# Kernel tuning notes

Hardware: AMD Instinct MI355X
Metric: run time of the kernel (lower is better)

Reference implementation:

```python
import jax, jax.numpy as jnp
import numpy as np

D = 256          # d_model
NH = 8           # n_heads
HD = D // NH
LEV = 3          # n_levels
NP = 4           # n_points
DFF = 1024       # d_ffn
B = 8            # batch
LQ = 3600        # 60*60 queries (hardcoded in get_reference_points)
SHAPES = np.array([[60, 60], [30, 30], [15, 15]], dtype=np.int64)
LIN = int((SHAPES[:, 0] * SHAPES[:, 1]).sum())  # 4725
START = np.concatenate([[0], np.cumsum(SHAPES[:, 0] * SHAPES[:, 1])[:-1]]).astype(np.int64)


def setup_inputs() -> dict:
    key = jax.random.key(0)
    ks = iter(jax.random.split(key, 32))
    def lin(k, o, i):
        return jax.random.normal(k, (o, i), jnp.float32) * 0.02
    return {
        "tgt": jax.random.normal(next(ks), (LQ, B, D), jnp.float32),
        "query_pos": jax.random.normal(next(ks), (1, 1, D), jnp.float32),
        "src": jax.random.normal(next(ks), (B, LIN, D), jnp.float32),
        "src_spatial_shapes": jnp.asarray(SHAPES),
        "level_start_index": jnp.asarray(START),
        "in_proj_w": lin(next(ks), 3 * D, D),
        "in_proj_b": jnp.zeros((3 * D,), jnp.float32),
        "out_proj_w": lin(next(ks), D, D),
        "out_proj_b": jnp.zeros((D,), jnp.float32),
        "samp_off_w": lin(next(ks), NH * LEV * NP * 2, D),
        "samp_off_b": jax.random.normal(next(ks), (NH * LEV * NP * 2,), jnp.float32) * 0.5,
        "attn_w_w": lin(next(ks), NH * LEV * NP, D),
        "attn_w_b": jnp.zeros((NH * LEV * NP,), jnp.float32),
        "value_proj_w": lin(next(ks), D, D),
        "value_proj_b": jnp.zeros((D,), jnp.float32),
        "cross_out_w": lin(next(ks), D, D),
        "cross_out_b": jnp.zeros((D,), jnp.float32),
        "ln1_g": jnp.ones((D,), jnp.float32), "ln1_b": jnp.zeros((D,), jnp.float32),
        "ln2_g": jnp.ones((D,), jnp.float32), "ln2_b": jnp.zeros((D,), jnp.float32),
        "ln3_g": jnp.ones((D,), jnp.float32), "ln3_b": jnp.zeros((D,), jnp.float32),
        "ffn_w1": lin(next(ks), DFF, D), "ffn_b1": jnp.zeros((DFF,), jnp.float32),
        "ffn_w2": lin(next(ks), D, DFF), "ffn_b2": jnp.zeros((D,), jnp.float32),
    }


def _ln(x, g, b, eps=1e-5):
    m = x.mean(-1, keepdims=True)
    v = ((x - m) ** 2).mean(-1, keepdims=True)
    return (x - m) * jax.lax.rsqrt(v + eps) * g + b


def _self_attn(q_in, k_in, v_in, wqkv, bqkv, wo, bo):
    # torch nn.MultiheadAttention semantics, inputs laid out (seq, batch, embed)
    S, N, _ = q_in.shape
    q = (q_in @ wqkv[:D].T + bqkv[:D]).reshape(S, N, NH, HD)
    k = (k_in @ wqkv[D:2 * D].T + bqkv[D:2 * D]).reshape(S, N, NH, HD)
    v = (v_in @ wqkv[2 * D:].T + bqkv[2 * D:]).reshape(S, N, NH, HD)
    logits = jnp.einsum('snhd,tnhd->nhst', q, k) / np.sqrt(HD).astype(np.float32)
    a = jax.nn.softmax(logits, -1)
    ctx = jnp.einsum('nhst,tnhd->snhd', a, v).reshape(S, N, D)
    return ctx @ wo.T + bo


def _bilinear(v_l, loc, Hl, Wl):
    # v_l: [B, NH, Hl*Wl, HD]; loc: [B, NH, LQ, NP, 2] normalized in [0,1]
    # grid_sample(align_corners=False, padding=zeros): pixel = loc*size - 0.5
    x = loc[..., 0] * Wl - 0.5
    y = loc[..., 1] * Hl - 0.5
    x0 = jnp.floor(x); y0 = jnp.floor(y)
    fx = x - x0; fy = y - y0
    x0 = x0.astype(jnp.int32); y0 = y0.astype(jnp.int32)
    def corner(yi, xi, w):
        valid = ((xi >= 0) & (xi < Wl) & (yi >= 0) & (yi < Hl)).astype(v_l.dtype)
        idx = jnp.clip(yi, 0, Hl - 1) * Wl + jnp.clip(xi, 0, Wl - 1)
        b, h, lq, p = idx.shape
        g = jnp.take_along_axis(v_l, idx.reshape(b, h, lq * p)[..., None], axis=2)
        return g.reshape(b, h, lq, p, HD) * (w * valid)[..., None]
    return (corner(y0, x0, (1 - fx) * (1 - fy))
            + corner(y0, x0 + 1, fx * (1 - fy))
            + corner(y0 + 1, x0, (1 - fx) * fy)
            + corner(y0 + 1, x0 + 1, fx * fy))


def _msdeform(query, ref, src, wso, bso, waw, baw, wv, bv, wo, bo):
    Bq, Lq, _ = query.shape
    value = (src @ wv.T + bv).reshape(Bq, LIN, NH, HD).transpose(0, 2, 1, 3)  # [B,NH,LIN,HD]
    off = (query @ wso.T + bso).reshape(Bq, Lq, NH, LEV, NP, 2)
    aw = (query @ waw.T + baw).reshape(Bq, Lq, NH, LEV * NP)
    aw = jax.nn.softmax(aw, -1).reshape(Bq, Lq, NH, LEV, NP)
    normalizer = jnp.asarray(SHAPES[:, ::-1].copy(), jnp.float32)  # (W, H) per level
    loc = ref[:, :, None, :, None, :] + off / normalizer[None, None, None, :, None, :]
    out = jnp.zeros((Bq, NH, Lq, HD), query.dtype)
    for l in range(LEV):
        Hl, Wl = int(SHAPES[l, 0]), int(SHAPES[l, 1])
        s = int(START[l])
        v_l = value[:, :, s:s + Hl * Wl]
        loc_l = loc[:, :, :, l].transpose(0, 2, 1, 3, 4)      # [B,NH,LQ,NP,2]
        sampled = _bilinear(v_l, loc_l, Hl, Wl)               # [B,NH,LQ,NP,HD]
        out = out + (sampled * aw[:, :, :, l].transpose(0, 2, 1, 3)[..., None]).sum(3)
    out = out.transpose(0, 2, 1, 3).reshape(Bq, Lq, D)
    return out @ wo.T + bo


def _reference_points():
    Hh = Ww = 60
    ys = (jnp.arange(Hh, dtype=jnp.float32) + 0.5) / Hh
    xs = (jnp.arange(Ww, dtype=jnp.float32) + 0.5) / Ww
    yy, xx = jnp.meshgrid(ys, xs, indexing='ij')
    ref = jnp.stack([xx.reshape(-1), yy.reshape(-1)], -1)[None]  # [1, 3600, 2]
    return jnp.broadcast_to(ref[:, :, None, :], (1, Hh * Ww, LEV, 2))


def reference(tgt, query_pos, src, src_spatial_shapes, level_start_index,
              in_proj_w, in_proj_b, out_proj_w, out_proj_b,
              samp_off_w, samp_off_b, attn_w_w, attn_w_b,
              value_proj_w, value_proj_b, cross_out_w, cross_out_b,
              ln1_g, ln1_b, ln2_g, ln2_b, ln3_g, ln3_b,
              ffn_w1, ffn_b1, ffn_w2, ffn_b2):
    # dropout layers are identity (eval mode). spatial shapes are static metadata
    # (SHAPES/START) since slicing sizes must be static under jit.
    q = (tgt + query_pos).transpose(1, 0, 2)
    tgt2 = _self_attn(q, q, tgt.transpose(1, 0, 2), in_proj_w, in_proj_b, out_proj_w, out_proj_b)
    t = _ln(tgt + tgt2.transpose(1, 0, 2), ln2_g, ln2_b)
    ref = _reference_points()
    tq = t.transpose(1, 0, 2)  # permute(1,0,2) -> [B, LQ, D]
    tgt2 = _msdeform(tq + query_pos, ref, src, samp_off_w, samp_off_b,
                     attn_w_w, attn_w_b, value_proj_w, value_proj_b,
                     cross_out_w, cross_out_b)
    tq = _ln(tq + tgt2, ln1_g, ln1_b)
    ff = jax.nn.relu(tq @ ffn_w1.T + ffn_b1) @ ffn_w2.T + ffn_b2
    tq = _ln(tq + ff, ln3_g, ln3_b)
    return tq.transpose(1, 0, 2)  # [LQ, B, D]
```

## Files before the change

kernel.cpp:

```cpp
#include <hip/hip_runtime.h>
#include <hip/hip_bf16.h>
#include <cstddef>
#include <cstdint>

#define D_MODEL 256
#define NHEAD   8
#define HDIM    32
#define NLEV    3
#define NPNT    4
#define DFF     1024
#define BATCH   8
#define LQ      3600
#define LIN     4725
#define MROWS   (BATCH*LQ)

typedef short bf16x8 __attribute__((ext_vector_type(8)));
typedef float f32x4  __attribute__((ext_vector_type(4)));

__device__ __forceinline__ unsigned short f2b(float x) {
    unsigned int u = __float_as_uint(x);
    unsigned int r = (u + 0x7fffu + ((u >> 16) & 1u)) >> 16;
    return (unsigned short)r;
}
__device__ __forceinline__ float b2f(unsigned short s) {
    return __uint_as_float(((unsigned int)s) << 16);
}

#define GLDS16(g, l) __builtin_amdgcn_global_load_lds( \
    (const __attribute__((address_space(1))) void*)(g), \
    (__attribute__((address_space(3))) void*)(l), 16, 0, 0)

#define WTOT 991232
__global__ __launch_bounds__(256) void prep_kernel(
    const float* __restrict__ tgt, unsigned short* __restrict__ tgtb,
    const float* __restrict__ srcf, unsigned short* __restrict__ srcb,
    const float* __restrict__ w_in, const float* __restrict__ w_out,
    const float* __restrict__ w_val, const float* __restrict__ w_cross,
    const float* __restrict__ w_so, const float* __restrict__ w_aw,
    const float* __restrict__ w_f1, const float* __restrict__ w_f2,
    unsigned short* __restrict__ wdst,
    const float* __restrict__ qp, const float* __restrict__ so_b,
    const float* __restrict__ aw_b, float* __restrict__ qpv)
{
    const int bid = blockIdx.x;
    const int tid = threadIdx.x;
    if (bid < 7200) {
        int i = bid * 256 + tid;
        float4 v = ((const float4*)tgt)[i];
        ushort4 o; o.x = f2b(v.x); o.y = f2b(v.y); o.z = f2b(v.z); o.w = f2b(v.w);
        ((ushort4*)tgtb)[i] = o;
    } else if (bid < 16650) {
        int i = (bid - 7200) * 256 + tid;
        float4 v = ((const float4*)srcf)[i];
        ushort4 o; o.x = f2b(v.x); o.y = f2b(v.y); o.z = f2b(v.z); o.w = f2b(v.w);
        ((ushort4*)srcb)[i] = o;
    } else if (bid < 17618) {
        int idx = ((bid - 16650) * 256 + tid) * 4;
        if (idx >= WTOT) return;
        const float* src; int off;
        if      (idx < 196608) { src = w_in;    off = idx; }
        else if (idx < 262144) { src = w_out;   off = idx - 196608; }
        else if (idx < 327680) { src = w_val;   off = idx - 262144; }
        else if (idx < 393216) { src = w_cross; off = idx - 327680; }
        else if (idx < 442368) { src = w_so;    off = idx - 393216; }
        else if (idx < 466944) { src = w_aw;    off = idx - 442368; }
        else if (idx < 729088) { src = w_f1;    off = idx - 466944; }
        else                   { src = w_f2;    off = idx - 729088; }
        float4 v = *(const float4*)(src + off);
        ushort4 o; o.x = f2b(v.x); o.y = f2b(v.y); o.z = f2b(v.z); o.w = f2b(v.w);
        *(ushort4*)(wdst + idx) = o;
    } else {
        int o = (bid - 17618) * 256 + tid;
        if (o >= 768 + 192 + 96) return;
        const float* wrow;
        if (o < 768)       wrow = w_in + (size_t)o * D_MODEL;
        else if (o < 960)  wrow = w_so + (size_t)(o - 768) * D_MODEL;
        else               wrow = w_aw + (size_t)(o - 960) * D_MODEL;
        float acc = 0.f;
        for (int d = 0; d < D_MODEL; ++d) acc += qp[d] * wrow[d];
        qpv[o] = acc;
        if (o >= 768) {
            float bias = (o < 960) ? so_b[o - 768] : aw_b[o - 960];
            qpv[1056 + (o - 768)] = acc + bias;
        }
    }
}

__global__ __launch_bounds__(256) void gemm_bf16(
    const unsigned short* __restrict__ A,
    const unsigned short* __restrict__ W,
    const float* __restrict__ bias,
    const float* __restrict__ bias2, int b2lim,
    float* __restrict__ Cf, unsigned short* __restrict__ Cb,
    int M, int N, int K, int relu)
{
    __shared__ __align__(16) unsigned short As[2 * 128 * 32];
    __shared__ __align__(16) unsigned short Bs[2 * 128 * 32];
    const int tid  = threadIdx.x;
    const int wave = tid >> 6;
    const int lane = tid & 63;
    const int m0 = blockIdx.x * 128;
    const int n0 = blockIdx.y * 128;

    const int lr  = lane >> 2;
    const int lc8 = (lane & 3) * 8;
    int ar0 = m0 + wave * 32 + lr;      if (ar0 > M - 1) ar0 = M - 1;
    int ar1 = m0 + wave * 32 + 16 + lr; if (ar1 > M - 1) ar1 = M - 1;
    int br0 = n0 + wave * 32 + lr;      if (br0 > N - 1) br0 = N - 1;
    int br1 = n0 + wave * 32 + 16 + lr; if (br1 > N - 1) br1 = N - 1;
    const unsigned short* pa0 = A + (size_t)ar0 * K + lc8;
    const unsigned short* pa1 = A + (size_t)ar1 * K + lc8;
    const unsigned short* pb0 = W + (size_t)br0 * K + lc8;
    const unsigned short* pb1 = W + (size_t)br1 * K + lc8;
    unsigned short* la0 = As + wave * 1024;
    unsigned short* la1 = As + wave * 1024 + 512;
    unsigned short* lb0 = Bs + wave * 1024;
    unsigned short* lb1 = Bs + wave * 1024 + 512;

    const int wm = (wave >> 1) * 64;
    const int wn = (wave & 1) * 64;
    const int fr = lane & 15;
    const int fk = (lane >> 4) * 8;

    f32x4 acc[4][4] = {};

    for (int k0 = 0; k0 < K; k0 += 64) {
        GLDS16(pa0, la0); GLDS16(pa0 + 32, la0 + 4096);
        GLDS16(pa1, la1); GLDS16(pa1 + 32, la1 + 4096);
        GLDS16(pb0, lb0); GLDS16(pb0 + 32, lb0 + 4096);
        GLDS16(pb1, lb1); GLDS16(pb1 + 32, lb1 + 4096);
        pa0 += 64; pa1 += 64; pb0 += 64; pb1 += 64;
        __syncthreads();
#pragma unroll
        for (int p = 0; p < 2; ++p) {
            bf16x8 af[4], bfv[4];
#pragma unroll
            for (int i = 0; i < 4; ++i)
                af[i] = *(const bf16x8*)&As[p * 4096 + (wm + i * 16 + fr) * 32 + fk];
#pragma unroll
            for (int j = 0; j < 4; ++j)
                bfv[j] = *(const bf16x8*)&Bs[p * 4096 + (wn + j * 16 + fr) * 32 + fk];
#pragma unroll
            for (int i = 0; i < 4; ++i)
#pragma unroll
                for (int j = 0; j < 4; ++j)
                    acc[i][j] = __builtin_amdgcn_mfma_f32_16x16x32_bf16(
                        af[i], bfv[j], acc[i][j], 0, 0, 0);
        }
        __syncthreads();
    }

    const int quad = lane >> 4;
#pragma unroll
    for (int j = 0; j < 4; ++j) {
        const int col = n0 + wn + j * 16 + fr;
        if (col >= N) continue;
        float bv = 0.f;
        if (bias) bv += bias[col];
        if (bias2 && col < b2lim) bv += bias2[col];
#pragma unroll
        for (int i = 0; i < 4; ++i) {
#pragma unroll
            for (int r = 0; r < 4; ++r) {
                const int row = m0 + wm + i * 16 + quad * 4 + r;
                if (row >= M) continue;
                float v = acc[i][j][r] + bv;
                if (relu) v = fmaxf(v, 0.f);
                if (Cf) Cf[(size_t)row * N + col] = v;
                if (Cb) Cb[(size_t)row * N + col] = f2b(v);
            }
        }
    }
}

__global__ __launch_bounds__(256) void gemm_ln(
    const unsigned short* __restrict__ A,
    const unsigned short* __restrict__ W,
    const float* __restrict__ bias,
    const float* __restrict__ resid,
    const float* __restrict__ g, const float* __restrict__ bb,
    float* __restrict__ outf, unsigned short* __restrict__ outb, int K)
{
    __shared__ __align__(16) unsigned short As[2 * 64 * 32];
    __shared__ __align__(16) unsigned short Bs[2 * 256 * 32];
    const int tid  = threadIdx.x;
    const int wave = tid >> 6;
    const int lane = tid & 63;
    const int m0 = blockIdx.x * 64;

    const int arow = tid >> 2;
    const int akc  = (tid & 3) * 8;
    const unsigned short* pa = A + (size_t)(m0 + arow) * K + akc;
    unsigned short* la = As + tid * 8;
    const unsigned short* pb0 = W + (size_t)(arow)       * K + akc;
    const unsigned short* pb1 = W + (size_t)(64  + arow) * K + akc;
    const unsigned short* pb2 = W + (size_t)(128 + arow) * K + akc;
    const unsigned short* pb3 = W + (size_t)(192 + arow) * K + akc;
    unsigned short* lb0 = Bs + tid * 8;
    unsigned short* lb1 = Bs + 2048 + tid * 8;
    unsigned short* lb2 = Bs + 4096 + tid * 8;
    unsigned short* lb3 = Bs + 6144 + tid * 8;

    const int fr = lane & 15;
    const int fk = (lane >> 4) * 8;
    const int quad = lane >> 4;
    const int colbase = wave * 64;

    f32x4 acc[4][4] = {};

    for (int k0 = 0; k0 < K; k0 += 64) {
        GLDS16(pa, la);        GLDS16(pa + 32, la + 2048);
        GLDS16(pb0, lb0);      GLDS16(pb0 + 32, lb0 + 8192);
        GLDS16(pb1, lb1);      GLDS16(pb1 + 32, lb1 + 8192);
        GLDS16(pb2, lb2);      GLDS16(pb2 + 32, lb2 + 8192);
        GLDS16(pb3, lb3);      GLDS16(pb3 + 32, lb3 + 8192);
        pa += 64; pb0 += 64; pb1 += 64; pb2 += 64; pb3 += 64;
        __syncthreads();
#pragma unroll
        for (int p = 0; p < 2; ++p) {
            bf16x8 af[4], bfv[4];
#pragma unroll
            for (int i = 0; i < 4; ++i)
                af[i] = *(const bf16x8*)&As[p * 2048 + (i * 16 + fr) * 32 + fk];
#pragma unroll
            for (int j = 0; j < 4; ++j)
                bfv[j] = *(const bf16x8*)&Bs[p * 8192 + (colbase + j * 16 + fr) * 32 + fk];
#pragma unroll
            for (int i = 0; i < 4; ++i)
#pragma unroll
                for (int j = 0; j < 4; ++j)
                    acc[i][j] = __builtin_amdgcn_mfma_f32_16x16x32_bf16(
                        af[i], bfv[j], acc[i][j], 0, 0, 0);
        }
        __syncthreads();
    }

    float2* red = (float2*)As;
    float rs[4][4], rq[4][4];
#pragma unroll
    for (int i = 0; i < 4; ++i) {
#pragma unroll
        for (int r = 0; r < 4; ++r) {
            const int row = m0 + i * 16 + quad * 4 + r;
            float s = 0.f, q = 0.f;
#pragma unroll
            for (int j = 0; j < 4; ++j) {
                const int col = colbase + j * 16 + fr;
                float v = acc[i][j][r] + bias[col] + resid[(size_t)row * 256 + col];
                acc[i][j][r] = v;
                s += v; q += v * v;
            }
            rs[i][r] = s; rq[i][r] = q;
        }
    }
#pragma unroll
    for (int off = 1; off < 16; off <<= 1) {
#pragma unroll
        for (int i = 0; i < 4; ++i)
#pragma unroll
            for (int r = 0; r < 4; ++r) {
                rs[i][r] += __shfl_xor(rs[i][r], off);
                rq[i][r] += __shfl_xor(rq[i][r], off);
            }
    }
    if ((lane & 15) == 0) {
#pragma unroll
        for (int i = 0; i < 4; ++i)
#pragma unroll
            for (int r = 0; r < 4; ++r)
                red[wave * 64 + i * 16 + quad * 4 + r] = make_float2(rs[i][r], rq[i][r]);
    }
    __syncthreads();
#pragma unroll
    for (int i = 0; i < 4; ++i) {
#pragma unroll
        for (int r = 0; r < 4; ++r) {
            const int rl = i * 16 + quad * 4 + r;
            const float2 t0 = red[rl], t1 = red[64 + rl], t2 = red[128 + rl], t3 = red[192 + rl];
            const float sum = t0.x + t1.x + t2.x + t3.x;
            const float sq  = t0.y + t1.y + t2.y + t3.y;
            const float mean = sum * (1.f / 256.f);
            const float var  = sq * (1.f / 256.f) - mean * mean;
            const float inv  = rsqrtf(var + 1e-5f);
            const int row = m0 + rl;
#pragma unroll
            for (int j = 0; j < 4; ++j) {
                const int col = colbase + j * 16 + fr;
                const float val = (acc[i][j][r] - mean) * inv * g[col] + bb[col];
                outf[(size_t)row * 256 + col] = val;
                if (outb) outb[(size_t)row * 256 + col] = f2b(val);
            }
        }
    }
}

__global__ __launch_bounds__(256) void self_attn_kernel(
    const unsigned short* __restrict__ qkv, unsigned short* __restrict__ ctx)
{
    __shared__ float sh[8][768];
    __shared__ float ls[8][8][8];
    const int n = blockIdx.x;
    const int t = threadIdx.x;
#pragma unroll
    for (int s = 0; s < 8; ++s) {
        const unsigned short* row = qkv + (size_t)(n * 8 + s) * 768;
        sh[s][t]       = b2f(row[t]);
        sh[s][t + 256] = b2f(row[t + 256]);
        sh[s][t + 512] = b2f(row[t + 512]);
    }
    __syncthreads();
    const int h = t >> 5, j = t & 31;
#pragma unroll
    for (int pair = j; pair < 64; pair += 32) {
        const int s = pair >> 3, tt = pair & 7;
        float acc = 0.f;
#pragma unroll
        for (int d = 0; d < 32; ++d)
            acc += sh[s][h * 32 + d] * sh[tt][256 + h * 32 + d];
        ls[h][s][tt] = acc * 0.17677669529663687f;
    }
    __syncthreads();
    if (t < 64) {
        const int hh = t >> 3, s = t & 7;
        float mx = -1e30f;
        for (int tt = 0; tt < 8; ++tt) mx = fmaxf(mx, ls[hh][s][tt]);
        float sum = 0.f;
        for (int tt = 0; tt < 8; ++tt) { float e = expf(ls[hh][s][tt] - mx); ls[hh][s][tt] = e; sum += e; }
        const float inv = 1.f / sum;
        for (int tt = 0; tt < 8; ++tt) ls[hh][s][tt] *= inv;
    }
    __syncthreads();
#pragma unroll
    for (int s = 0; s < 8; ++s) {
        float acc = 0.f;
#pragma unroll
        for (int tt = 0; tt < 8; ++tt)
            acc += ls[h][s][tt] * sh[tt][512 + h * 32 + j];
        ctx[(size_t)(n * 8 + s) * D_MODEL + h * 32 + j] = f2b(acc);
    }
}

__global__ __launch_bounds__(256) void msprep_kernel(float* __restrict__ comb)
{
    const int tid = threadIdx.x;
    const int m = blockIdx.x * 32 + (tid >> 3);
    const int h = tid & 7;
    const int lq = m >> 3;
    const float* offp = comb + (size_t)m * 288 + h * 24;
    const float* awp  = comb + (size_t)m * 288 + 192 + h * 12;
    float off[24], aw[12];
#pragma unroll
    for (int i = 0; i < 6; ++i) *(float4*)&off[i * 4] = ((const float4*)offp)[i];
#pragma unroll
    for (int i = 0; i < 3; ++i) *(float4*)&aw[i * 4] = ((const float4*)awp)[i];

    float mx = aw[0];
#pragma unroll
    for (int i = 1; i < 12; ++i) mx = fmaxf(mx, aw[i]);
    float se = 0.f;
#pragma unroll
    for (int i = 0; i < 12; ++i) { aw[i] = __expf(aw[i] - mx); se += aw[i]; }
    const float inv = 1.f / se;

    const float refx = ((lq % 60) + 0.5f) * (1.f / 60.f);
    const float refy = ((lq / 60) + 0.5f) * (1.f / 60.f);
    const int HW[3] = {60, 30, 15};
    const int ST[3] = {0, 3600, 4500};

    unsigned int outv[36];
#pragma unroll
    for (int lev = 0; lev < NLEV; ++lev) {
        const int Wl = HW[lev], Hl = HW[lev], s0 = ST[lev];
        const float fWl = (float)Wl, fHl = (float)Hl;
#pragma unroll
        for (int p = 0; p < NPNT; ++p) {
            const int pt = lev * 4 + p;
            const float ox = off[lev * 8 + p * 2];
            const float oy = off[lev * 8 + p * 2 + 1];
            const float px = refx * fWl + ox - 0.5f;
            const float py = refy * fHl + oy - 0.5f;
            const float x0f = floorf(px), y0f = floorf(py);
            const float fx = px - x0f, fy = py - y0f;
            const int x0 = (int)x0f, y0 = (int)y0f;
            const float aww = aw[pt] * inv;
            const float vx0 = (x0 >= 0 && x0 < Wl) ? 1.f : 0.f;
            const float vx1 = (x0 >= -1 && x0 < Wl - 1) ? 1.f : 0.f;
            const float vy0 = (y0 >= 0 && y0 < Hl) ? 1.f : 0.f;
            const float vy1 = (y0 >= -1 && y0 < Hl - 1) ? 1.f : 0.f;
            const int xc0 = min(max(x0, 0), Wl - 1);
            const int xc1 = min(max(x0 + 1, 0), Wl - 1);
            const int yc0 = min(max(y0, 0), Hl - 1);
            const int yc1 = min(max(y0 + 1, 0), Hl - 1);
            const unsigned int sx  = (unsigned int)(xc1 - xc0);
            const unsigned int syW = (unsigned int)((yc1 - yc0) * Wl);
            const unsigned int idx = (unsigned int)(s0 + yc0 * Wl + xc0);
            const float w00 = (1.f - fx) * (1.f - fy) * aww * vx0 * vy0;
            const float w01 = fx * (1.f - fy) * aww * vx1 * vy0;
            const float w10 = (1.f - fx) * fy * aww * vx0 * vy1;
            const float w11 = fx * fy * aww * vx1 * vy1;
            outv[pt * 3]     = idx | (sx << 16) | (syW << 17);
            outv[pt * 3 + 1] = (unsigned int)f2b(w00) | ((unsigned int)f2b(w01) << 16);
            outv[pt * 3 + 2] = (unsigned int)f2b(w10) | ((unsigned int)f2b(w11) << 16);
        }
    }
    __syncthreads();
    uint4* dst = (uint4*)((char*)comb + (size_t)m * 1152 + h * 144);
#pragma unroll
    for (int i = 0; i < 9; ++i) dst[i] = *(uint4*)&outv[i * 4];
}

__global__ __launch_bounds__(256) void msdeform_kernel(
    const unsigned short* __restrict__ value,
    const unsigned int* __restrict__ meta,
    unsigned short* __restrict__ out)
{
    const int bid = blockIdx.x;
    const int b   = bid & 7;
    const int lq0 = (bid >> 3) * 4;
    const int r    = threadIdx.x >> 6;
    const int lane = threadIdx.x & 63;
    const int h = lane >> 3;
    const int l = lane & 7;
    const int m = (lq0 + r) * 8 + b;

    const unsigned int* mp = meta + (size_t)m * 288 + h * 36;
    uint4 md[9];
#pragma unroll
    for (int i = 0; i < 9; ++i) md[i] = ((const uint4*)mp)[i];
    const unsigned int* mw = (const unsigned int*)md;

    const unsigned short* vbase = value + (size_t)b * LIN * 256 + h * 32 + l * 4;

    float a0 = 0.f, a1 = 0.f, a2 = 0.f, a3 = 0.f;
#pragma unroll
    for (int p = 0; p < 12; ++p) {
        const unsigned int pack = mw[p * 3];
        const unsigned int wlo  = mw[p * 3 + 1];
        const unsigned int whi  = mw[p * 3 + 2];
        const unsigned int i00 = pack & 0xFFFFu;
        const unsigned int sx  = (pack >> 16) & 1u;
        const unsigned int syW = pack >> 17;
        const unsigned int i01 = i00 + sx;
        const unsigned int i10 = i00 + syW;
        const unsigned int i11 = i10 + sx;
        const float w00 = __uint_as_float(wlo << 16);
        const float w01 = __uint_as_float(wlo & 0xFFFF0000u);
        const float w10 = __uint_as_float(whi << 16);
        const float w11 = __uint_as_float(whi & 0xFFFF0000u);
        const ushort4 g00 = *(const ushort4*)(vbase + (size_t)i00 * 256);
        const ushort4 g01 = *(const ushort4*)(vbase + (size_t)i01 * 256);
        const ushort4 g10 = *(const ushort4*)(vbase + (size_t)i10 * 256);
        const ushort4 g11 = *(const ushort4*)(vbase + (size_t)i11 * 256);
        a0 += b2f(g00.x) * w00 + b2f(g01.x) * w01 + b2f(g10.x) * w10 + b2f(g11.x) * w11;
        a1 += b2f(g00.y) * w00 + b2f(g01.y) * w01 + b2f(g10.y) * w10 + b2f(g11.y) * w11;
        a2 += b2f(g00.z) * w00 + b2f(g01.z) * w01 + b2f(g10.z) * w10 + b2f(g11.z) * w11;
        a3 += b2f(g00.w) * w00 + b2f(g01.w) * w01 + b2f(g10.w) * w10 + b2f(g11.w) * w11;
    }
    ushort4 o;
    o.x = f2b(a0); o.y = f2b(a1); o.z = f2b(a2); o.w = f2b(a3);
    *(ushort4*)(out + (size_t)m * 256 + h * 32 + l * 4) = o;
}

extern "C" void kernel_launch(void* const* d_in, const int* in_sizes, int n_in,
                              void* d_out, int out_size, void* d_ws, size_t ws_size,
                              hipStream_t stream)
{
    (void)in_sizes; (void)n_in; (void)out_size; (void)ws_size;
    const float* tgt          = (const float*)d_in[0];
    const float* qp           = (const float*)d_in[1];
    const float* src          = (const float*)d_in[2];
    const float* in_proj_w    = (const float*)d_in[5];
    const float* in_proj_b    = (const float*)d_in[6];
    const float* out_proj_w   = (const float*)d_in[7];
    const float* out_proj_b   = (const float*)d_in[8];
    const float* samp_off_w   = (const float*)d_in[9];
    const float* samp_off_b   = (const float*)d_in[10];
    const float* attn_w_w     = (const float*)d_in[11];
    const float* attn_w_b     = (const float*)d_in[12];
    const float* value_proj_w = (const float*)d_in[13];
    const float* value_proj_b = (const float*)d_in[14];
    const float* cross_out_w  = (const float*)d_in[15];
    const float* cross_out_b  = (const float*)d_in[16];
    const float* ln1_g = (const float*)d_in[17];
    const float* ln1_b = (const float*)d_in[18];
    const float* ln2_g = (const float*)d_in[19];
    const float* ln2_b = (const float*)d_in[20];
    const float* ln3_g = (const float*)d_in[21];
    const float* ln3_b = (const float*)d_in[22];
    const float* ffn_w1 = (const float*)d_in[23];
    const float* ffn_b1 = (const float*)d_in[24];
    const float* ffn_w2 = (const float*)d_in[25];
    const float* ffn_b2 = (const float*)d_in[26];
    float* out = (float*)d_out;

    float* ws    = (float*)d_ws;
    float* t     = ws;
    float* t2    = ws + 7372800;
    float* comb  = ws + 14745600;
    float* qpv   = ws + 23040000;
    float* cbias = qpv + 1056;

    unsigned short* bws    = (unsigned short*)((char*)d_ws + 92165376);
    unsigned short* s1     = bws;
    unsigned short* tgtb   = s1;
    unsigned short* ctxb   = s1;
    unsigned short* tb     = s1;
    unsigned short* t2b    = s1;
    unsigned short* s2     = bws + 7372800;
    unsigned short* qkvb   = s2;
    unsigned short* valueb = s2;
    unsigned short* msoutb = s2 + 9676800;
    unsigned short* hiddenb= s2;
    unsigned short* srcb   = bws + 36864000;
    unsigned short* wtsb   = bws + 46540800;

    prep_kernel<<<17623, 256, 0, stream>>>(tgt, tgtb, src, srcb,
                                           in_proj_w, out_proj_w, value_proj_w,
                                           cross_out_w, samp_off_w, attn_w_w,
                                           ffn_w1, ffn_w2, wtsb,
                                           qp, samp_off_b, attn_w_b, qpv);
    gemm_bf16<<<dim3(225, 6), 256, 0, stream>>>(tgtb, wtsb + 0, in_proj_b, qpv, 512,
                                                nullptr, qkvb, MROWS, 768, 256, 0);
    self_attn_kernel<<<3600, 256, 0, stream>>>(qkvb, ctxb);
    gemm_ln<<<450, 256, 0, stream>>>(ctxb, wtsb + 196608, out_proj_b, tgt,
                                     ln2_g, ln2_b, t, tb, 256);
    gemm_bf16<<<dim3(296, 2), 256, 0, stream>>>(srcb, wtsb + 262144, value_proj_b, nullptr, 0,
                                                nullptr, valueb, BATCH * LIN, 256, 256, 0);
    gemm_bf16<<<dim3(225, 3), 256, 0, stream>>>(tb, wtsb + 393216, cbias, nullptr, 0,
                                                comb, nullptr, MROWS, 288, 256, 0);
    msprep_kernel<<<900, 256, 0, stream>>>(comb);
    msdeform_kernel<<<7200, 256, 0, stream>>>(valueb, (const unsigned int*)comb, msoutb);
    gemm_ln<<<450, 256, 0, stream>>>(msoutb, wtsb + 327680, cross_out_b, t,
                                     ln1_g, ln1_b, t2, t2b, 256);
    gemm_bf16<<<dim3(225, 8), 256, 0, stream>>>(t2b, wtsb + 466944, ffn_b1, nullptr, 0,
                                                nullptr, hiddenb, MROWS, DFF, 256, 1);
    gemm_ln<<<450, 256, 0, stream>>>(hiddenb, wtsb + 729088, ffn_b2, t2,
                                     ln3_g, ln3_b, out, nullptr, 1024);
}
```

Measured before the change: 472.6 us.

## Replace global_load_lds with register-prefetched double-buffered LDS pipeline in GEMMs

Both GEMM kernels drop the direct global-to-LDS loads and instead prefetch the next K-slice into registers while computing on the current LDS buffer, then write to a ping-pong LDS buffer with explicit waitcnt and barriers. The LayerNorm-fused GEMM also halves its row tile from 64 to 32, doubling its grid to 900 blocks for more parallelism. This aims to overlap global memory latency with MFMA work. The cost is more registers and extra LDS store instructions, and the smaller LN tile reloads the full 256-column weight tile per 32 rows, doubling weight traffic.

```diff
diff --git a/kernel.cpp b/kernel.cpp
--- a/kernel.cpp
+++ b/kernel.cpp
@@ -26,9 +26,8 @@
     return __uint_as_float(((unsigned int)s) << 16);
 }
 
-#define GLDS16(g, l) __builtin_amdgcn_global_load_lds( \
-    (const __attribute__((address_space(1))) void*)(g), \
-    (__attribute__((address_space(3))) void*)(l), 16, 0, 0)
+#define WAIT_LGKM0() __builtin_amdgcn_s_waitcnt(0xC07F)
+#define BARRIER()    __builtin_amdgcn_s_barrier()
 
 #define WTOT 991232
 __global__ __launch_bounds__(256) void prep_kernel(
@@ -94,60 +93,72 @@
     float* __restrict__ Cf, unsigned short* __restrict__ Cb,
     int M, int N, int K, int relu)
 {
-    __shared__ __align__(16) unsigned short As[2 * 128 * 32];
-    __shared__ __align__(16) unsigned short Bs[2 * 128 * 32];
+    __shared__ __align__(16) unsigned short As[2][4096];
+    __shared__ __align__(16) unsigned short Bs[2][4096];
     const int tid  = threadIdx.x;
     const int wave = tid >> 6;
     const int lane = tid & 63;
     const int m0 = blockIdx.x * 128;
     const int n0 = blockIdx.y * 128;
 
-    const int lr  = lane >> 2;
-    const int lc8 = (lane & 3) * 8;
-    int ar0 = m0 + wave * 32 + lr;      if (ar0 > M - 1) ar0 = M - 1;
-    int ar1 = m0 + wave * 32 + 16 + lr; if (ar1 > M - 1) ar1 = M - 1;
-    int br0 = n0 + wave * 32 + lr;      if (br0 > N - 1) br0 = N - 1;
-    int br1 = n0 + wave * 32 + 16 + lr; if (br1 > N - 1) br1 = N - 1;
-    const unsigned short* pa0 = A + (size_t)ar0 * K + lc8;
-    const unsigned short* pa1 = A + (size_t)ar1 * K + lc8;
-    const unsigned short* pb0 = W + (size_t)br0 * K + lc8;
-    const unsigned short* pb1 = W + (size_t)br1 * K + lc8;
-    unsigned short* la0 = As + wave * 1024;
-    unsigned short* la1 = As + wave * 1024 + 512;
-    unsigned short* lb0 = Bs + wave * 1024;
-    unsigned short* lb1 = Bs + wave * 1024 + 512;
+    int arow = m0 + (tid >> 1); if (arow > M - 1) arow = M - 1;
+    int brow = n0 + (tid >> 1); if (brow > N - 1) brow = N - 1;
+    const unsigned short* pa = A + (size_t)arow * K + (tid & 1) * 16;
+    const unsigned short* pb = W + (size_t)brow * K + (tid & 1) * 16;
+    const int soff = tid * 16;
 
     const int wm = (wave >> 1) * 64;
     const int wn = (wave & 1) * 64;
     const int fr = lane & 15;
     const int fk = (lane >> 4) * 8;
 
+    const int NI = K >> 5;
     f32x4 acc[4][4] = {};
 
-    for (int k0 = 0; k0 < K; k0 += 64) {
-        GLDS16(pa0, la0); GLDS16(pa0 + 32, la0 + 4096);
-        GLDS16(pa1, la1); GLDS16(pa1 + 32, la1 + 4096);
-        GLDS16(pb0, lb0); GLDS16(pb0 + 32, lb0 + 4096);
-        GLDS16(pb1, lb1); GLDS16(pb1 + 32, lb1 + 4096);
-        pa0 += 64; pa1 += 64; pb0 += 64; pb1 += 64;
-        __syncthreads();
-#pragma unroll
-        for (int p = 0; p < 2; ++p) {
-            bf16x8 af[4], bfv[4];
-#pragma unroll
-            for (int i = 0; i < 4; ++i)
-                af[i] = *(const bf16x8*)&As[p * 4096 + (wm + i * 16 + fr) * 32 + fk];
-#pragma unroll
-            for (int j = 0; j < 4; ++j)
-                bfv[j] = *(const bf16x8*)&Bs[p * 4096 + (wn + j * 16 + fr) * 32 + fk];
-#pragma unroll
-            for (int i = 0; i < 4; ++i)
-#pragma unroll
-                for (int j = 0; j < 4; ++j)
-                    acc[i][j] = __builtin_amdgcn_mfma_f32_16x16x32_bf16(
-                        af[i], bfv[j], acc[i][j], 0, 0, 0);
-        }
-        __syncthreads();
+    uint4 ra0, ra1, rb0, rb1;
+    uint4 sa0, sa1, sb0, sb1;
+    ra0 = *(const uint4*)(pa);     ra1 = *(const uint4*)(pa + 8);
+    rb0 = *(const uint4*)(pb);     rb1 = *(const uint4*)(pb + 8);
+
+    auto compute = [&](int buf) {
+        bf16x8 af[4], bfv[4];
+#pragma unroll
+        for (int x = 0; x < 4; ++x)
+            af[x] = *(const bf16x8*)&As[buf][(wm + x * 16 + fr) * 32 + fk];
+#pragma unroll
+        for (int y = 0; y < 4; ++y)
+            bfv[y] = *(const bf16x8*)&Bs[buf][(wn + y * 16 + fr) * 32 + fk];
+#pragma unroll
+        for (int x = 0; x < 4; ++x)
+#pragma unroll
+            for (int y = 0; y < 4; ++y)
+                acc[x][y] = __builtin_amdgcn_mfma_f32_16x16x32_bf16(
+                    af[x], bfv[y], acc[x][y], 0, 0, 0);
+    };
+
+    for (int i = 0; i < NI; i += 2) {
+        {
+            const unsigned short* qa = pa + (size_t)(i + 1) * 32;
+            const unsigned short* qb = pb + (size_t)(i + 1) * 32;
+            sa0 = *(const uint4*)(qa); sa1 = *(const uint4*)(qa + 8);
+            sb0 = *(const uint4*)(qb); sb1 = *(const uint4*)(qb + 8);
+        }
+        *(uint4*)&As[0][soff] = ra0; *(uint4*)&As[0][soff + 8] = ra1;
+        *(uint4*)&Bs[0][soff] = rb0; *(uint4*)&Bs[0][soff + 8] = rb1;
+        WAIT_LGKM0(); BARRIER();
+        compute(0);
+        BARRIER();
+        if (i + 2 < NI) {
+            const unsigned short* qa = pa + (size_t)(i + 2) * 32;
+            const unsigned short* qb = pb + (size_t)(i + 2) * 32;
+            ra0 = *(const uint4*)(qa); ra1 = *(const uint4*)(qa + 8);
+            rb0 = *(const uint4*)(qb); rb1 = *(const uint4*)(qb + 8);
+        }
+        *(uint4*)&As[1][soff] = sa0; *(uint4*)&As[1][soff + 8] = sa1;
+        *(uint4*)&Bs[1][soff] = sb0; *(uint4*)&Bs[1][soff + 8] = sb1;
+        WAIT_LGKM0(); BARRIER();
+        compute(1);
+        BARRIER();
     }
 
     const int quad = lane >> 4;
@@ -181,102 +192,119 @@
     const float* __restrict__ g, const float* __restrict__ bb,
     float* __restrict__ outf, unsigned short* __restrict__ outb, int K)
 {
-    __shared__ __align__(16) unsigned short As[2 * 64 * 32];
-    __shared__ __align__(16) unsigned short Bs[2 * 256 * 32];
+    __shared__ __align__(16) unsigned short As[2][1024];
+    __shared__ __align__(16) unsigned short Bs[2][8192];
     const int tid  = threadIdx.x;
     const int wave = tid >> 6;
     const int lane = tid & 63;
-    const int m0 = blockIdx.x * 64;
-
-    const int arow = tid >> 2;
-    const int akc  = (tid & 3) * 8;
-    const unsigned short* pa = A + (size_t)(m0 + arow) * K + akc;
-    unsigned short* la = As + tid * 8;
-    const unsigned short* pb0 = W + (size_t)(arow)       * K + akc;
-    const unsigned short* pb1 = W + (size_t)(64  + arow) * K + akc;
-    const unsigned short* pb2 = W + (size_t)(128 + arow) * K + akc;
-    const unsigned short* pb3 = W + (size_t)(192 + arow) * K + akc;
-    unsigned short* lb0 = Bs + tid * 8;
-    unsigned short* lb1 = Bs + 2048 + tid * 8;
-    unsigned short* lb2 = Bs + 4096 + tid * 8;
-    unsigned short* lb3 = Bs + 6144 + tid * 8;
+    const int m0 = blockIdx.x * 32;
+
+    const bool doA = (tid < 128);
+    const unsigned short* pa = A + (size_t)(m0 + (tid >> 2)) * K + (tid & 3) * 8;
+    const unsigned short* pb0 = W + (size_t)(tid >> 2) * K + (tid & 3) * 8;
+    const unsigned short* pb1 = pb0 + (size_t)64 * K;
+    const unsigned short* pb2 = pb0 + (size_t)128 * K;
+    const unsigned short* pb3 = pb0 + (size_t)192 * K;
+    const int so = tid * 8;
 
     const int fr = lane & 15;
     const int fk = (lane >> 4) * 8;
     const int quad = lane >> 4;
     const int colbase = wave * 64;
-
-    f32x4 acc[4][4] = {};
-
-    for (int k0 = 0; k0 < K; k0 += 64) {
-        GLDS16(pa, la);        GLDS16(pa + 32, la + 2048);
-        GLDS16(pb0, lb0);      GLDS16(pb0 + 32, lb0 + 8192);
-        GLDS16(pb1, lb1);      GLDS16(pb1 + 32, lb1 + 8192);
-        GLDS16(pb2, lb2);      GLDS16(pb2 + 32, lb2 + 8192);
-        GLDS16(pb3, lb3);      GLDS16(pb3 + 32, lb3 + 8192);
-        pa += 64; pb0 += 64; pb1 += 64; pb2 += 64; pb3 += 64;
-        __syncthreads();
-#pragma unroll
-        for (int p = 0; p < 2; ++p) {
-            bf16x8 af[4], bfv[4];
-#pragma unroll
-            for (int i = 0; i < 4; ++i)
-                af[i] = *(const bf16x8*)&As[p * 2048 + (i * 16 + fr) * 32 + fk];
-#pragma unroll
-            for (int j = 0; j < 4; ++j)
-                bfv[j] = *(const bf16x8*)&Bs[p * 8192 + (colbase + j * 16 + fr) * 32 + fk];
-#pragma unroll
-            for (int i = 0; i < 4; ++i)
-#pragma unroll
-                for (int j = 0; j < 4; ++j)
-                    acc[i][j] = __builtin_amdgcn_mfma_f32_16x16x32_bf16(
-                        af[i], bfv[j], acc[i][j], 0, 0, 0);
-        }
-        __syncthreads();
-    }
-
-    float2* red = (float2*)As;
-    float rs[4][4], rq[4][4];
-#pragma unroll
-    for (int i = 0; i < 4; ++i) {
+    const int NI = K >> 5;
+
+    f32x4 acc[2][4] = {};
+    uint4 ra, rb0, rb1, rb2, rb3;
+    uint4 sa, sb0, sb1, sb2, sb3;
+    if (doA) ra = *(const uint4*)(pa);
+    rb0 = *(const uint4*)(pb0); rb1 = *(const uint4*)(pb1);
+    rb2 = *(const uint4*)(pb2); rb3 = *(const uint4*)(pb3);
+
+    auto compute = [&](int buf) {
+        bf16x8 af[2], bfv[4];
+#pragma unroll
+        for (int x = 0; x < 2; ++x)
+            af[x] = *(const bf16x8*)&As[buf][(x * 16 + fr) * 32 + fk];
+#pragma unroll
+        for (int y = 0; y < 4; ++y)
+            bfv[y] = *(const bf16x8*)&Bs[buf][(colbase + y * 16 + fr) * 32 + fk];
+#pragma unroll
+        for (int x = 0; x < 2; ++x)
+#pragma unroll
+            for (int y = 0; y < 4; ++y)
+                acc[x][y] = __builtin_amdgcn_mfma_f32_16x16x32_bf16(
+                    af[x], bfv[y], acc[x][y], 0, 0, 0);
+    };
+
+    for (int i = 0; i < NI; i += 2) {
+        {
+            const int k1 = (i + 1) * 32;
+            if (doA) sa = *(const uint4*)(pa + k1);
+            sb0 = *(const uint4*)(pb0 + k1); sb1 = *(const uint4*)(pb1 + k1);
+            sb2 = *(const uint4*)(pb2 + k1); sb3 = *(const uint4*)(pb3 + k1);
+        }
+        if (doA) *(uint4*)&As[0][so] = ra;
+        *(uint4*)&Bs[0][so] = rb0;        *(uint4*)&Bs[0][2048 + so] = rb1;
+        *(uint4*)&Bs[0][4096 + so] = rb2; *(uint4*)&Bs[0][6144 + so] = rb3;
+        WAIT_LGKM0(); BARRIER();
+        compute(0);
+        BARRIER();
+        if (i + 2 < NI) {
+            const int k2 = (i + 2) * 32;
+            if (doA) ra = *(const uint4*)(pa + k2);
+            rb0 = *(const uint4*)(pb0 + k2); rb1 = *(const uint4*)(pb1 + k2);
+            rb2 = *(const uint4*)(pb2 + k2); rb3 = *(const uint4*)(pb3 + k2);
+        }
+        if (doA) *(uint4*)&As[1][so] = sa;
+        *(uint4*)&Bs[1][so] = sb0;        *(uint4*)&Bs[1][2048 + so] = sb1;
+        *(uint4*)&Bs[1][4096 + so] = sb2; *(uint4*)&Bs[1][6144 + so] = sb3;
+        WAIT_LGKM0(); BARRIER();
+        compute(1);
+        BARRIER();
+    }
+
+    float2* red = (float2*)&As[0][0];
+    float rs[2][4], rq[2][4];
+#pragma unroll
+    for (int x = 0; x < 2; ++x) {
 #pragma unroll
         for (int r = 0; r < 4; ++r) {
-            const int row = m0 + i * 16 + quad * 4 + r;
+            const int row = m0 + x * 16 + quad * 4 + r;
             float s = 0.f, q = 0.f;
 #pragma unroll
-            for (int j = 0; j < 4; ++j) {
-                const int col = colbase + j * 16 + fr;
-                float v = acc[i][j][r] + bias[col] + resid[(size_t)row * 256 + col];
-                acc[i][j][r] = v;
+            for (int y = 0; y < 4; ++y) {
+                const int col = colbase + y * 16 + fr;
+                float v = acc[x][y][r] + bias[col] + resid[(size_t)row * 256 + col];
+                acc[x][y][r] = v;
                 s += v; q += v * v;
             }
-            rs[i][r] = s; rq[i][r] = q;
+            rs[x][r] = s; rq[x][r] = q;
         }
     }
 #pragma unroll
     for (int off = 1; off < 16; off <<= 1) {
 #pragma unroll
-        for (int i = 0; i < 4; ++i)
+        for (int x = 0; x < 2; ++x)
 #pragma unroll
             for (int r = 0; r < 4; ++r) {
-                rs[i][r] += __shfl_xor(rs[i][r], off);
-                rq[i][r] += __shfl_xor(rq[i][r], off);
+                rs[x][r] += __shfl_xor(rs[x][r], off);
+                rq[x][r] += __shfl_xor(rq[x][r], off);
             }
     }
     if ((lane & 15) == 0) {
 #pragma unroll
-        for (int i = 0; i < 4; ++i)
+        for (int x = 0; x < 2; ++x)
 #pragma unroll
             for (int r = 0; r < 4; ++r)
-                red[wave * 64 + i * 16 + quad * 4 + r] = make_float2(rs[i][r], rq[i][r]);
+                red[wave * 32 + x * 16 + quad * 4 + r] = make_float2(rs[x][r], rq[x][r]);
     }
     __syncthreads();
 #pragma unroll
-    for (int i = 0; i < 4; ++i) {
+    for (int x = 0; x < 2; ++x) {
 #pragma unroll
         for (int r = 0; r < 4; ++r) {
-            const int rl = i * 16 + quad * 4 + r;
-            const float2 t0 = red[rl], t1 = red[64 + rl], t2 = red[128 + rl], t3 = red[192 + rl];
+            const int rl = x * 16 + quad * 4 + r;
+            const float2 t0 = red[rl], t1 = red[32 + rl], t2 = red[64 + rl], t3 = red[96 + rl];
             const float sum = t0.x + t1.x + t2.x + t3.x;
             const float sq  = t0.y + t1.y + t2.y + t3.y;
             const float mean = sum * (1.f / 256.f);
@@ -284,9 +312,9 @@
             const float inv  = rsqrtf(var + 1e-5f);
             const int row = m0 + rl;
 #pragma unroll
-            for (int j = 0; j < 4; ++j) {
-                const int col = colbase + j * 16 + fr;
-                const float val = (acc[i][j][r] - mean) * inv * g[col] + bb[col];
+            for (int y = 0; y < 4; ++y) {
+                const int col = colbase + y * 16 + fr;
+                const float val = (acc[x][y][r] - mean) * inv * g[col] + bb[col];
                 outf[(size_t)row * 256 + col] = val;
                 if (outb) outb[(size_t)row * 256 + col] = f2b(val);
             }
@@ -522,7 +550,7 @@
     gemm_bf16<<<dim3(225, 6), 256, 0, stream>>>(tgtb, wtsb + 0, in_proj_b, qpv, 512,
                                                 nullptr, qkvb, MROWS, 768, 256, 0);
     self_attn_kernel<<<3600, 256, 0, stream>>>(qkvb, ctxb);
-    gemm_ln<<<450, 256, 0, stream>>>(ctxb, wtsb + 196608, out_proj_b, tgt,
+    gemm_ln<<<900, 256, 0, stream>>>(ctxb, wtsb + 196608, out_proj_b, tgt,
                                      ln2_g, ln2_b, t, tb, 256);
     gemm_bf16<<<dim3(296, 2), 256, 0, stream>>>(srcb, wtsb + 262144, value_proj_b, nullptr, 0,
                                                 nullptr, valueb, BATCH * LIN, 256, 256, 0);
@@ -530,10 +558,10 @@
                                                 comb, nullptr, MROWS, 288, 256, 0);
     msprep_kernel<<<900, 256, 0, stream>>>(comb);
     msdeform_kernel<<<7200, 256, 0, stream>>>(valueb, (const unsigned int*)comb, msoutb);
-    gemm_ln<<<450, 256, 0, stream>>>(msoutb, wtsb + 327680, cross_out_b, t,
+    gemm_ln<<<900, 256, 0, stream>>>(msoutb, wtsb + 327680, cross_out_b, t,
                                      ln1_g, ln1_b, t2, t2b, 256);
     gemm_bf16<<<dim3(225, 8), 256, 0, stream>>>(t2b, wtsb + 466944, ffn_b1, nullptr, 0,
                                                 nullptr, hiddenb, MROWS, DFF, 256, 1);
-    gemm_ln<<<450, 256, 0, stream>>>(hiddenb, wtsb + 729088, ffn_b2, t2,
+    gemm_ln<<<900, 256, 0, stream>>>(hiddenb, wtsb + 729088, ffn_b2, t2,
                                      ln3_g, ln3_b, out, nullptr, 1024);
 }
```

Result: slower. 513.3 us (+8.6%).

## Fuse FFN up-projection, ReLU, down-projection and LayerNorm into one kernel

Applied to the files above, without the earlier changes.

Replaces the FFN1 GEMM plus the FFN2 GEMM+LN pair with a single kernel. Each block handles 32 rows and walks the 1024-wide hidden dimension in 64-column chunks, keeping the ReLU'd hidden activations in shared memory instead of writing and re-reading a bf16 hidden tensor through global memory. The cost is that every block reloads the full W1 and W2 weights, and the 32-row tiles with frequent syncs lower MFMA reuse and occupancy compared with the separate GEMMs.

```diff
diff --git a/kernel.cpp b/kernel.cpp
--- a/kernel.cpp
+++ b/kernel.cpp
@@ -294,6 +294,151 @@
     }
 }
 
+__global__ __launch_bounds__(256) void ffn_fused_kernel(
+    const unsigned short* __restrict__ A,
+    const unsigned short* __restrict__ W1,
+    const float* __restrict__ b1,
+    const unsigned short* __restrict__ W2,
+    const float* __restrict__ b2,
+    const float* __restrict__ resid,
+    const float* __restrict__ g, const float* __restrict__ bb,
+    float* __restrict__ outf)
+{
+    __shared__ __align__(16) unsigned short Ab[8192];
+    __shared__ __align__(16) unsigned short Wc[16384];
+    __shared__ __align__(16) unsigned short hid[2048];
+    __shared__ float2 red[128];
+    const int tid  = threadIdx.x;
+    const int wave = tid >> 6;
+    const int lane = tid & 63;
+    const int m0 = blockIdx.x * 32;
+    const int fr   = lane & 15;
+    const int quad = lane >> 4;
+    const int fk   = quad * 8;
+
+#pragma unroll
+    for (int j = 0; j < 4; ++j) {
+        const int c = wave * 4 + j;
+        GLDS16(A + (size_t)(m0 + c * 2 + (lane >> 5)) * 256 + (lane & 31) * 8,
+               Ab + c * 512);
+    }
+    __syncthreads();
+    bf16x8 af[2][8];
+#pragma unroll
+    for (int i = 0; i < 2; ++i)
+#pragma unroll
+        for (int s = 0; s < 8; ++s)
+            af[i][s] = *(const bf16x8*)&Ab[(i * 16 + fr) * 256 + s * 32 + fk];
+
+    f32x4 acc2[2][4] = {};
+
+    for (int h = 0; h < 16; ++h) {
+        __syncthreads();
+#pragma unroll
+        for (int j = 0; j < 8; ++j) {
+            const int c = wave * 8 + j;
+            GLDS16(W1 + (size_t)(h * 64 + c * 2 + (lane >> 5)) * 256 + (lane & 31) * 8,
+                   Wc + c * 512);
+        }
+        __syncthreads();
+        f32x4 acc1[2] = {};
+#pragma unroll
+        for (int s = 0; s < 8; ++s) {
+            bf16x8 bv = *(const bf16x8*)&Wc[(wave * 16 + fr) * 256 + s * 32 + fk];
+            acc1[0] = __builtin_amdgcn_mfma_f32_16x16x32_bf16(af[0][s], bv, acc1[0], 0, 0, 0);
+            acc1[1] = __builtin_amdgcn_mfma_f32_16x16x32_bf16(af[1][s], bv, acc1[1], 0, 0, 0);
+        }
+        const float bias1 = b1[h * 64 + wave * 16 + fr];
+#pragma unroll
+        for (int i = 0; i < 2; ++i)
+#pragma unroll
+            for (int r = 0; r < 4; ++r) {
+                float v = fmaxf(acc1[i][r] + bias1, 0.f);
+                hid[(i * 16 + quad * 4 + r) * 64 + wave * 16 + fr] = f2b(v);
+            }
+        __syncthreads();
+#pragma unroll
+        for (int j = 0; j < 8; ++j) {
+            const int c = wave * 8 + j;
+            GLDS16(W2 + (size_t)(c * 8 + (lane >> 3)) * 1024 + h * 64 + (lane & 7) * 8,
+                   Wc + c * 512);
+        }
+        __syncthreads();
+#pragma unroll
+        for (int s = 0; s < 2; ++s) {
+            bf16x8 a2[2], b2v[4];
+#pragma unroll
+            for (int i = 0; i < 2; ++i)
+                a2[i] = *(const bf16x8*)&hid[(i * 16 + fr) * 64 + s * 32 + fk];
+#pragma unroll
+            for (int j2 = 0; j2 < 4; ++j2)
+                b2v[j2] = *(const bf16x8*)&Wc[(wave * 64 + j2 * 16 + fr) * 64 + s * 32 + fk];
+#pragma unroll
+            for (int i = 0; i < 2; ++i)
+#pragma unroll
+                for (int j2 = 0; j2 < 4; ++j2)
+                    acc2[i][j2] = __builtin_amdgcn_mfma_f32_16x16x32_bf16(
+                        a2[i], b2v[j2], acc2[i][j2], 0, 0, 0);
+        }
+    }
+
+    const int colbase = wave * 64;
+    float rs[2][4], rq[2][4];
+#pragma unroll
+    for (int x = 0; x < 2; ++x) {
+#pragma unroll
+        for (int r = 0; r < 4; ++r) {
+            const int row = m0 + x * 16 + quad * 4 + r;
+            float s = 0.f, q = 0.f;
+#pragma unroll
+            for (int y = 0; y < 4; ++y) {
+                const int col = colbase + y * 16 + fr;
+                float v = acc2[x][y][r] + b2[col] + resid[(size_t)row * 256 + col];
+                acc2[x][y][r] = v;
+                s += v; q += v * v;
+            }
+            rs[x][r] = s; rq[x][r] = q;
+        }
+    }
+#pragma unroll
+    for (int off = 1; off < 16; off <<= 1) {
+#pragma unroll
+        for (int x = 0; x < 2; ++x)
+#pragma unroll
+            for (int r = 0; r < 4; ++r) {
+                rs[x][r] += __shfl_xor(rs[x][r], off);
+                rq[x][r] += __shfl_xor(rq[x][r], off);
+            }
+    }
+    if ((lane & 15) == 0) {
+#pragma unroll
+        for (int x = 0; x < 2; ++x)
+#pragma unroll
+            for (int r = 0; r < 4; ++r)
+                red[wave * 32 + x * 16 + quad * 4 + r] = make_float2(rs[x][r], rq[x][r]);
+    }
+    __syncthreads();
+#pragma unroll
+    for (int x = 0; x < 2; ++x) {
+#pragma unroll
+        for (int r = 0; r < 4; ++r) {
+            const int rl = x * 16 + quad * 4 + r;
+            const float2 t0 = red[rl], t1 = red[32 + rl], t2 = red[64 + rl], t3 = red[96 + rl];
+            const float sum = t0.x + t1.x + t2.x + t3.x;
+            const float sq  = t0.y + t1.y + t2.y + t3.y;
+            const float mean = sum * (1.f / 256.f);
+            const float var  = sq * (1.f / 256.f) - mean * mean;
+            const float inv  = rsqrtf(var + 1e-5f);
+            const int row = m0 + rl;
+#pragma unroll
+            for (int y = 0; y < 4; ++y) {
+                const int col = colbase + y * 16 + fr;
+                outf[(size_t)row * 256 + col] = (acc2[x][y][r] - mean) * inv * g[col] + bb[col];
+            }
+        }
+    }
+}
+
 __global__ __launch_bounds__(256) void self_attn_kernel(
     const unsigned short* __restrict__ qkv, unsigned short* __restrict__ ctx)
 {
@@ -510,7 +655,6 @@
     unsigned short* qkvb   = s2;
     unsigned short* valueb = s2;
     unsigned short* msoutb = s2 + 9676800;
-    unsigned short* hiddenb= s2;
     unsigned short* srcb   = bws + 36864000;
     unsigned short* wtsb   = bws + 46540800;
 
@@ -532,8 +676,7 @@
     msdeform_kernel<<<7200, 256, 0, stream>>>(valueb, (const unsigned int*)comb, msoutb);
     gemm_ln<<<450, 256, 0, stream>>>(msoutb, wtsb + 327680, cross_out_b, t,
                                      ln1_g, ln1_b, t2, t2b, 256);
-    gemm_bf16<<<dim3(225, 8), 256, 0, stream>>>(t2b, wtsb + 466944, ffn_b1, nullptr, 0,
-                                                nullptr, hiddenb, MROWS, DFF, 256, 1);
-    gemm_ln<<<450, 256, 0, stream>>>(hiddenb, wtsb + 729088, ffn_b2, t2,
-                                     ln3_g, ln3_b, out, nullptr, 1024);
-}
+    ffn_fused_kernel<<<900, 256, 0, stream>>>(t2b, wtsb + 466944, ffn_b1,
+                                              wtsb + 729088, ffn_b2, t2,
+                                              ln3_g, ln3_b, out);
+}
```

After: 486.9 us. 1.03x slower.
